# Performance work log

Hardware: AMD Instinct MI355X
Metric: run time of the kernel (lower is better)

## Reference

```python
import jax, jax.numpy as jnp
import numpy as np

N = 524288          # number of query points
L_FREQ = 16         # frequencies in positional encoding -> dim_encoding = 3*2*16 = 96
DIM_ENC = 96
DIM_HID = 128
NUM_LAYERS = 8      # 1 input layer + 7 hidden layers + 1 output layer
DIM_OUT = 4
DIM_IN_HID = DIM_HID + DIM_ENC  # concat skip: 224


def setup_inputs() -> dict:
    key = jax.random.key(0)
    ks = jax.random.split(key, 7)
    def lin(k, fan_in, shape):
        return jax.random.uniform(k, shape, jnp.float32, -1.0, 1.0) / np.sqrt(fan_in)
    return {
        "query_points": jax.random.uniform(ks[0], (N, 3), jnp.float32),
        "W0": lin(ks[1], DIM_ENC, (DIM_ENC, DIM_HID)),
        "b0": lin(ks[2], DIM_ENC, (DIM_HID,)),
        "Wh": lin(ks[3], DIM_IN_HID, (NUM_LAYERS - 1, DIM_IN_HID, DIM_HID)),
        "bh": lin(ks[4], DIM_IN_HID, (NUM_LAYERS - 1, DIM_HID)),
        "Wl": lin(ks[5], DIM_IN_HID, (DIM_IN_HID, DIM_OUT)),
        "bl": lin(ks[6], DIM_IN_HID, (DIM_OUT,)),
    }


def _encode(x):
    # NeRF frequency encoding: [N,3] -> [N, 3*2*L_FREQ]
    freqs = (2.0 ** jnp.arange(L_FREQ, dtype=x.dtype)) * jnp.pi
    xf = x[..., None] * freqs                      # [N, 3, L]
    enc = jnp.concatenate([jnp.sin(xf), jnp.cos(xf)], axis=-1)  # [N, 3, 2L]
    return enc.reshape(x.shape[0], -1)             # [N, 96]


def reference(query_points, W0, b0, Wh, bh, Wl, bl):
    enc = _encode(query_points)                    # [N, 96]
    outs = jnp.maximum(enc @ W0 + b0, 0.0)         # [N, 128]
    outs = jnp.concatenate([outs, enc], axis=-1)   # concat skip -> [N, 224]
    for i in range(Wh.shape[0]):                   # 7 structurally-distinct hidden layers
        outs = jnp.maximum(outs @ Wh[i] + bh[i], 0.0)
        outs = jnp.concatenate([outs, enc], axis=-1)
    return outs @ Wl + bl                          # [N, 4], no activation on last layer
```

## Files before the change

### kernel.cpp

```cpp
#include <hip/hip_runtime.h>
#include <stdint.h>

typedef unsigned short u16;
typedef __bf16 bf16x8 __attribute__((ext_vector_type(8)));
typedef float f32x4 __attribute__((ext_vector_type(4)));
typedef float f32x16 __attribute__((ext_vector_type(16)));
typedef unsigned int u32;

#define IMG_H(l) (14336 + ((l)-1) * 30720)
#define IMG_OUT 229376
#define IMG_TOTAL 237056

__device__ inline int fmap(int k) {
    int s = k >> 4, h = (k >> 3) & 1, j = k & 7;
    return 32 * (s >> 1) + 16 * (s & 1) + 8 * (j >> 2) + 4 * h + (j & 3);
}
__device__ inline u16 b16rne(float v) {
    u32 u = __builtin_bit_cast(u32, v);
    u += 0x7FFFu + ((u >> 16) & 1u);
    return (u16)(u >> 16);
}

__global__ void nf_prep(const float* __restrict__ W0, const float* __restrict__ b0,
                        const float* __restrict__ Wh, const float* __restrict__ bh,
                        const float* __restrict__ Wl, const float* __restrict__ bl,
                        u16* __restrict__ img) {
    int idx = blockIdx.x * 256 + threadIdx.x;
    if (idx >= IMG_TOTAL) return;
    float v;
    if (idx < 14336) {
        int gg = idx >> 3, j = idx & 7;
        int koct = gg >> 7, i = gg & 127, k = koct * 8 + j;
        v = (k < 96) ? W0[k * 128 + i] : (k == 96) ? b0[i] : 0.f;
    } else if (idx < IMG_OUT) {
        int r = idx - 14336, l = r / 30720, rr = r % 30720;
        int gg = rr >> 3, j = rr & 7;
        int koct = gg >> 7, i = gg & 127, k = koct * 8 + j;
        const float* W = Wh + l * 224 * 128;
        v = (k < 128) ? W[fmap(k) * 128 + i]
          : (k < 224) ? W[k * 128 + i]
          : (k == 224) ? bh[l * 128 + i] : 0.f;
    } else {
        int r = idx - IMG_OUT;
        int gg = r >> 3, j = r & 7;
        int koct = gg >> 5, i = gg & 31, k = koct * 8 + j;
        v = 0.f;
        if (i < 4)
            v = (k < 128) ? Wl[fmap(k) * 4 + i]
              : (k < 224) ? Wl[k * 4 + i]
              : (k == 224) ? bl[i] : 0.f;
    }
    img[idx] = b16rne(v);
}

__device__ inline f32x16 MF32(bf16x8 a, bf16x8 b, f32x16 c) {
    return __builtin_amdgcn_mfma_f32_32x32x16_bf16(a, b, c, 0, 0, 0);
}
__device__ inline bf16x8 fr4(const u32 (&p)[4]) {
    union { u32 u[4]; bf16x8 v; } x;
    x.u[0] = p[0]; x.u[1] = p[1]; x.u[2] = p[2]; x.u[3] = p[3];
    return x.v;
}
__device__ inline bf16x8 frCB(u32 c0) {
    union { u32 u[4]; bf16x8 v; } x;
    x.u[0] = c0; x.u[1] = 0; x.u[2] = 0; x.u[3] = 0;
    return x.v;
}
__device__ inline bf16x8 ldA(const u16* base, int gi) {
    union { uint4 q; bf16x8 v; } x;
    x.q = *(const uint4*)(base + (gi << 3));
    return x.v;
}
__device__ inline u32 pkbf(float a, float b) {
    u32 ua = __builtin_bit_cast(u32, a) + 0x8000u;
    u32 ub = __builtin_bit_cast(u32, b) + 0x8000u;
    return __builtin_amdgcn_perm(ub, ua, 0x07060302u);
}
template<int BYTES>
__device__ inline void stageT(const u16* gsrc, u16* ldst, int wave, int lane) {
    const char* gs = (const char*)gsrc + lane * 16;
    char* ls = (char*)ldst;
    constexpr int TRIPS = (BYTES + 4095) / 4096;
#pragma unroll
    for (int i = 0; i < TRIPS; i++) {
        const int c = wave * 1024 + i * 4096;
        if ((BYTES % 4096) == 0 || i < TRIPS - 1 || c < BYTES)
            __builtin_amdgcn_global_load_lds(
                (const __attribute__((address_space(1))) void*)(gs + c),
                (__attribute__((address_space(3))) void*)(ls + c), 16, 0, 0);
    }
}
__device__ inline void zeroacc(f32x16 (&acc)[4][2]) {
#pragma unroll
    for (int t = 0; t < 4; t++)
#pragma unroll
        for (int n = 0; n < 2; n++)
#pragma unroll
            for (int r = 0; r < 16; r++) acc[t][n][r] = 0.f;
}
__device__ inline void bh_t(const f32x16 (&acc)[4][2], u32 (&H)[2][8][4], int t) {
#pragma unroll
    for (int n = 0; n < 2; n++)
#pragma unroll
        for (int hf = 0; hf < 2; hf++) {
            const int s = 2 * t + hf, rb = hf * 8;
#pragma unroll
            for (int q = 0; q < 4; q++)
                H[n][s][q] = pkbf(fmaxf(acc[t][n][rb + 2 * q], 0.f),
                                  fmaxf(acc[t][n][rb + 2 * q + 1], 0.f));
        }
}
__device__ inline void buildH(const f32x16 (&acc)[4][2], u32 (&H)[2][8][4]) {
#pragma unroll
    for (int t = 0; t < 4; t++) bh_t(acc, H, t);
}

#define WAITV(N) asm volatile("s_waitcnt vmcnt(" #N ")" ::: "memory")
#define BAR() do { __builtin_amdgcn_s_barrier(); \
                   __builtin_amdgcn_sched_barrier(0x2 | 0x4 | 0x8); } while (0)

__device__ inline void mmRow(const u16* A, int h, int m32, int s,
                             bf16x8 B0, bf16x8 B1, f32x16 (&acc)[4][2]) {
#pragma unroll
    for (int t = 0; t < 4; t++) {
        bf16x8 a = ldA(A, (2 * s + h) * 128 + t * 32 + m32);
        acc[t][0] = MF32(a, B0, acc[t][0]);
        acc[t][1] = MF32(a, B1, acc[t][1]);
    }
}
__device__ inline void mmOne(const u16* A, int h, int m32, int s, int t,
                             bf16x8 B0, bf16x8 B1, f32x16 (&acc)[4][2]) {
    bf16x8 a = ldA(A, (2 * s + h) * 128 + t * 32 + m32);
    acc[t][0] = MF32(a, B0, acc[t][0]);
    acc[t][1] = MF32(a, B1, acc[t][1]);
}

__device__ inline void cH04(const u16* A, int h, int m32, f32x16 (&acc)[4][2],
                            const u32 (&H)[2][8][4]) {
    __builtin_amdgcn_s_setprio(1);
#pragma unroll
    for (int s = 0; s < 5; s++)
        mmRow(A, h, m32, s, fr4(H[0][s]), fr4(H[1][s]), acc);
    __builtin_amdgcn_s_setprio(0);
}
__device__ inline void cH57E0(const u16* A, int h, int m32, f32x16 (&acc)[4][2],
                              const u32 (&H)[2][8][4], const u32 (&E)[2][3][2][4]) {
    __builtin_amdgcn_s_setprio(1);
    mmRow(A, h, m32, 0, fr4(H[0][5]), fr4(H[1][5]), acc);
    mmRow(A, h, m32, 1, fr4(H[0][6]), fr4(H[1][6]), acc);
    mmRow(A, h, m32, 2, fr4(H[0][7]), fr4(H[1][7]), acc);
    mmRow(A, h, m32, 3, fr4(E[0][0][0]), fr4(E[1][0][0]), acc);
    mmRow(A, h, m32, 4, fr4(E[0][0][1]), fr4(E[1][0][1]), acc);
    __builtin_amdgcn_s_setprio(0);
}
__device__ inline void cE12b_tp(const u16* A, int h, int m32, f32x16 (&acc)[4][2],
                                const u32 (&E)[2][3][2][4], u32 CB0,
                                u32 (&H)[2][8][4]) {
    __builtin_amdgcn_s_setprio(1);
    const bf16x8 cb = frCB(CB0);
#pragma unroll
    for (int p = 0; p < 2; p++) {
        const int t0 = 2 * p, t1 = 2 * p + 1;
#pragma unroll
        for (int s = 0; s < 5; s++) {
            bf16x8 B0, B1;
            if (s < 4) { B0 = fr4(E[0][1 + (s >> 1)][s & 1]);
                         B1 = fr4(E[1][1 + (s >> 1)][s & 1]); }
            else       { B0 = cb; B1 = cb; }
            mmOne(A, h, m32, s, t0, B0, B1, acc);
            mmOne(A, h, m32, s, t1, B0, B1, acc);
        }
        bh_t(acc, H, t0);
        bh_t(acc, H, t1);
    }
    __builtin_amdgcn_s_setprio(0);
}
__device__ inline void cL0a(const u16* A, int h, int m32, f32x16 (&acc)[4][2],
                            const u32 (&E)[2][3][2][4]) {
    __builtin_amdgcn_s_setprio(1);
#pragma unroll
    for (int s = 0; s < 5; s++)
        mmRow(A, h, m32, s, fr4(E[0][s >> 1][s & 1]), fr4(E[1][s >> 1][s & 1]), acc);
    __builtin_amdgcn_s_setprio(0);
}
__device__ inline void cL0b(const u16* A, int h, int m32, f32x16 (&acc)[4][2],
                            const u32 (&E)[2][3][2][4], u32 CB0) {
    __builtin_amdgcn_s_setprio(1);
    mmRow(A, h, m32, 0, fr4(E[0][2][1]), fr4(E[1][2][1]), acc);
    mmRow(A, h, m32, 1, frCB(CB0), frCB(CB0), acc);
    __builtin_amdgcn_s_setprio(0);
}

__global__ __launch_bounds__(256, 2) void nf_main(const float* __restrict__ qp,
                                                  const u16* __restrict__ img,
                                                  float* __restrict__ out) {
    __shared__ alignas(16) u16 lds[3][10240];
    const int tid = threadIdx.x, wave = tid >> 6, lane = tid & 63;
    const int m32 = lane & 31, h = lane >> 5;
    const int pbase = blockIdx.x * 256 + wave * 64;

    stageT<20480>(img, &lds[0][0], wave, lane);
    stageT<8192>(img + 10240, &lds[1][0], wave, lane);

    u32 E[2][3][2][4];
    const float sc0 = h ? 128.0f : 0.5f;
#pragma unroll
    for (int n = 0; n < 2; n++)
#pragma unroll
        for (int c = 0; c < 3; c++) {
            float r = qp[(pbase + n * 32 + m32) * 3 + c] * sc0;
            float sn[8], cs[8];
#pragma unroll
            for (int t = 0; t < 8; t++) {
                float fr = __builtin_amdgcn_fractf(r);
                sn[t] = __builtin_amdgcn_sinf(fr);
                cs[t] = __builtin_amdgcn_cosf(fr);
                r = r * 2.0f;
            }
#pragma unroll
            for (int q = 0; q < 4; q++) {
                E[n][c][0][q] = pkbf(sn[2 * q], sn[2 * q + 1]);
                E[n][c][1][q] = pkbf(cs[2 * q], cs[2 * q + 1]);
            }
        }
    const u32 CB0 = (h == 0) ? 0x00003F80u : 0u;

    f32x16 acc[4][2];
    u32 H[2][8][4];
    zeroacc(acc);

    WAITV(2); BAR();
    stageT<20480>(img + IMG_H(1), &lds[2][0], wave, lane);
    cL0a(&lds[0][0], h, m32, acc, E);
    WAITV(5); BAR();
    stageT<20480>(img + IMG_H(1) + 10240, &lds[0][0], wave, lane);
    cL0b(&lds[1][0], h, m32, acc, E, CB0);
    buildH(acc, H);
    WAITV(5); BAR();

#pragma unroll 1
    for (int l = 1; l < 8; l++) {
        const int base = IMG_H(l);
        stageT<20480>(img + base + 20480, &lds[1][0], wave, lane);
        zeroacc(acc);
        cH04(&lds[2][0], h, m32, acc, H);
        WAITV(5); BAR();
        if (l < 7) {
            stageT<20480>(img + IMG_H(l + 1), &lds[2][0], wave, lane);
        } else {
            stageT<15360>(img + IMG_OUT, &lds[2][0], wave, lane);
        }
        cH57E0(&lds[0][0], h, m32, acc, H, E);
        if (l < 7) { WAITV(5); } else { WAITV(3); }
        BAR();
        if (l < 7)
            stageT<20480>(img + IMG_H(l + 1) + 10240, &lds[0][0], wave, lane);
        cE12b_tp(&lds[1][0], h, m32, acc, E, CB0, H);
        if (l < 7) { WAITV(5); } else { WAITV(0); }
        BAR();
    }

    f32x16 o0, o1;
#pragma unroll
    for (int r = 0; r < 16; r++) { o0[r] = 0.f; o1[r] = 0.f; }
    __builtin_amdgcn_s_setprio(1);
#pragma unroll
    for (int s = 0; s < 15; s++) {
        bf16x8 B0, B1;
        if (s < 8)       { B0 = fr4(H[0][s]); B1 = fr4(H[1][s]); }
        else if (s < 14) { B0 = fr4(E[0][(s - 8) >> 1][(s - 8) & 1]);
                           B1 = fr4(E[1][(s - 8) >> 1][(s - 8) & 1]); }
        else             { B0 = frCB(CB0); B1 = B0; }
        bf16x8 a = ldA(&lds[2][0], (2 * s + h) * 32 + m32);
        o0 = MF32(a, B0, o0);
        o1 = MF32(a, B1, o1);
    }
    __builtin_amdgcn_s_setprio(0);
    if (h == 0) {
        f32x4 w0 = {o0[0], o0[1], o0[2], o0[3]};
        f32x4 w1 = {o1[0], o1[1], o1[2], o1[3]};
        *(f32x4*)(out + 4 * (pbase + m32)) = w0;
        *(f32x4*)(out + 4 * (pbase + 32 + m32)) = w1;
    }
}

extern "C" void kernel_launch(void* const* d_in, const int* in_sizes, int n_in,
                              void* d_out, int out_size, void* d_ws, size_t ws_size,
                              hipStream_t stream) {
    const float* qp = (const float*)d_in[0];
    const float* W0 = (const float*)d_in[1];
    const float* b0 = (const float*)d_in[2];
    const float* Wh = (const float*)d_in[3];
    const float* bh = (const float*)d_in[4];
    const float* Wl = (const float*)d_in[5];
    const float* bl = (const float*)d_in[6];
    float* out = (float*)d_out;
    u16* img = (u16*)d_ws;

    nf_prep<<<926, 256, 0, stream>>>(W0, b0, Wh, bh, Wl, bl, img);
    nf_main<<<2048, 256, 0, stream>>>(qp, img, out);
}
```

Baseline: 277.3 us.

## Stagger block start, use runtime-trip staging loop, narrow setprio scope, full sched barrier

Replaces the templated unrolled LDS staging helper with a runtime-bounded loop, and makes BAR a full scheduling barrier. Narrows the high-priority window in the last MFMA phase so the bf16 pack work runs at normal priority. Adds an s_sleep for alternating blocks to stagger their start and spread out contention for global memory. The runtime loop may generate extra scalar control code, and the hard-coded vmcnt waits assume a fixed number of outstanding loads per wave.

```diff
diff --git a/kernel.cpp b/kernel.cpp
--- a/kernel.cpp
+++ b/kernel.cpp
@@ -76,19 +76,13 @@
     u32 ub = __builtin_bit_cast(u32, b) + 0x8000u;
     return __builtin_amdgcn_perm(ub, ua, 0x07060302u);
 }
-template<int BYTES>
-__device__ inline void stageT(const u16* gsrc, u16* ldst, int wave, int lane) {
+__device__ inline void stageA(const u16* gsrc, u16* ldst, int bytes, int wave, int lane) {
     const char* gs = (const char*)gsrc + lane * 16;
     char* ls = (char*)ldst;
-    constexpr int TRIPS = (BYTES + 4095) / 4096;
-#pragma unroll
-    for (int i = 0; i < TRIPS; i++) {
-        const int c = wave * 1024 + i * 4096;
-        if ((BYTES % 4096) == 0 || i < TRIPS - 1 || c < BYTES)
-            __builtin_amdgcn_global_load_lds(
-                (const __attribute__((address_space(1))) void*)(gs + c),
-                (__attribute__((address_space(3))) void*)(ls + c), 16, 0, 0);
-    }
+    for (int c = wave * 1024; c < bytes; c += 4096)
+        __builtin_amdgcn_global_load_lds(
+            (const __attribute__((address_space(1))) void*)(gs + c),
+            (__attribute__((address_space(3))) void*)(ls + c), 16, 0, 0);
 }
 __device__ inline void zeroacc(f32x16 (&acc)[4][2]) {
 #pragma unroll
@@ -116,8 +110,7 @@
 }
 
 #define WAITV(N) asm volatile("s_waitcnt vmcnt(" #N ")" ::: "memory")
-#define BAR() do { __builtin_amdgcn_s_barrier(); \
-                   __builtin_amdgcn_sched_barrier(0x2 | 0x4 | 0x8); } while (0)
+#define BAR() do { __builtin_amdgcn_s_barrier(); __builtin_amdgcn_sched_barrier(0); } while (0)
 
 __device__ inline void mmRow(const u16* A, int h, int m32, int s,
                              bf16x8 B0, bf16x8 B1, f32x16 (&acc)[4][2]) {
@@ -156,11 +149,11 @@
 __device__ inline void cE12b_tp(const u16* A, int h, int m32, f32x16 (&acc)[4][2],
                                 const u32 (&E)[2][3][2][4], u32 CB0,
                                 u32 (&H)[2][8][4]) {
-    __builtin_amdgcn_s_setprio(1);
     const bf16x8 cb = frCB(CB0);
 #pragma unroll
     for (int p = 0; p < 2; p++) {
         const int t0 = 2 * p, t1 = 2 * p + 1;
+        __builtin_amdgcn_s_setprio(1);
 #pragma unroll
         for (int s = 0; s < 5; s++) {
             bf16x8 B0, B1;
@@ -170,10 +163,10 @@
             mmOne(A, h, m32, s, t0, B0, B1, acc);
             mmOne(A, h, m32, s, t1, B0, B1, acc);
         }
+        __builtin_amdgcn_s_setprio(0);
         bh_t(acc, H, t0);
         bh_t(acc, H, t1);
     }
-    __builtin_amdgcn_s_setprio(0);
 }
 __device__ inline void cL0a(const u16* A, int h, int m32, f32x16 (&acc)[4][2],
                             const u32 (&E)[2][3][2][4]) {
@@ -199,8 +192,10 @@
     const int m32 = lane & 31, h = lane >> 5;
     const int pbase = blockIdx.x * 256 + wave * 64;
 
-    stageT<20480>(img, &lds[0][0], wave, lane);
-    stageT<8192>(img + 10240, &lds[1][0], wave, lane);
+    if ((blockIdx.x ^ (blockIdx.x >> 8)) & 1) __builtin_amdgcn_s_sleep(10);
+
+    stageA(img, &lds[0][0], 20480, wave, lane);
+    stageA(img + 10240, &lds[1][0], 8192, wave, lane);
 
     u32 E[2][3][2][4];
     const float sc0 = h ? 128.0f : 0.5f;
@@ -230,10 +225,10 @@
     zeroacc(acc);
 
     WAITV(2); BAR();
-    stageT<20480>(img + IMG_H(1), &lds[2][0], wave, lane);
+    stageA(img + IMG_H(1), &lds[2][0], 20480, wave, lane);
     cL0a(&lds[0][0], h, m32, acc, E);
     WAITV(5); BAR();
-    stageT<20480>(img + IMG_H(1) + 10240, &lds[0][0], wave, lane);
+    stageA(img + IMG_H(1) + 10240, &lds[0][0], 20480, wave, lane);
     cL0b(&lds[1][0], h, m32, acc, E, CB0);
     buildH(acc, H);
     WAITV(5); BAR();
@@ -241,20 +236,17 @@
 #pragma unroll 1
     for (int l = 1; l < 8; l++) {
         const int base = IMG_H(l);
-        stageT<20480>(img + base + 20480, &lds[1][0], wave, lane);
+        stageA(img + base + 20480, &lds[1][0], 20480, wave, lane);
         zeroacc(acc);
         cH04(&lds[2][0], h, m32, acc, H);
         WAITV(5); BAR();
-        if (l < 7) {
-            stageT<20480>(img + IMG_H(l + 1), &lds[2][0], wave, lane);
-        } else {
-            stageT<15360>(img + IMG_OUT, &lds[2][0], wave, lane);
-        }
+        const u16* nsrc = (l < 7) ? (img + IMG_H(l + 1)) : (img + IMG_OUT);
+        stageA(nsrc, &lds[2][0], (l < 7) ? 20480 : 15360, wave, lane);
         cH57E0(&lds[0][0], h, m32, acc, H, E);
         if (l < 7) { WAITV(5); } else { WAITV(3); }
         BAR();
         if (l < 7)
-            stageT<20480>(img + IMG_H(l + 1) + 10240, &lds[0][0], wave, lane);
+            stageA(img + IMG_H(l + 1) + 10240, &lds[0][0], 20480, wave, lane);
         cE12b_tp(&lds[1][0], h, m32, acc, E, CB0, H);
         if (l < 7) { WAITV(5); } else { WAITV(0); }
         BAR();
```

Result: no change. 282.1 us (+1.7%).
